# Kernel tuning notes

Measured on AMD Instinct MI355X. Metric: run time of the kernel, lower is better.

The kernel has to match this reference:

```python
import jax, jax.numpy as jnp
import numpy as np

B, W, F, N = 256, 512, 512, 512


def setup_inputs() -> dict:
    key = jax.random.key(0)
    k1, k2, k3, k4, k5 = jax.random.split(key, 5)
    return {
        "x": jax.random.normal(k1, (B, W, F), dtype=jnp.float32),
        "weight_k": jax.random.normal(k2, (F, N), dtype=jnp.float32),
        "weight_q": jax.random.normal(k3, (F, N), dtype=jnp.float32),
        "weight_v": jax.random.normal(k4, (F, N), dtype=jnp.float32),
        "w": jax.random.normal(k5, (W, 1), dtype=jnp.float32),
    }


def reference(x, weight_k, weight_q, weight_v, w):
    # x: (B, W, F)
    n_outputs = weight_k.shape[-1]
    # Per-word K/V projections (original loops over words; here one batched GEMM)
    K = jnp.einsum("bwf,fn->bwn", x, weight_k)  # (B, W, N)
    V = jnp.einsum("bwf,fn->bwn", x, weight_v)  # (B, W, N)
    # Per-sample query: t = x^T @ w -> (F,), q = t @ weight_q -> (N,)
    t = jnp.einsum("bwf,w->bf", x, w[:, 0])     # (B, F)
    Q = t @ weight_q                              # (B, N)
    # Scores over words, scaled, softmax across the word axis
    scores = jnp.einsum("bn,bwn->bw", Q, K) / jnp.sqrt(jnp.float32(n_outputs))
    weights = jax.nn.softmax(scores, axis=1)      # (B, W)
    # Weighted sum of V over words
    return jnp.einsum("bw,bwn->bn", weights, V)   # (B, N)
```

## Files before the change

### kernel.cpp

```cpp
#include <hip/hip_runtime.h>
#include <math.h>

#define B 256
#define W 512
#define F 512
#define N 512
#define GPART 4
#define WPG (W / GPART)

__global__ __launch_bounds__(512) void tpart_kernel(
    const float* __restrict__ x,
    const float* __restrict__ wvec,
    float* __restrict__ t_part)
{
    const int blk = blockIdx.x;
    const int g   = blk & (GPART - 1);
    const int b   = blk >> 2;
    const int tid = threadIdx.x;
    const int ws  = tid >> 7;
    const int f4  = tid & 127;

    __shared__ float s_w[WPG];
    __shared__ float s_part[4][F];

    if (tid < WPG) s_w[tid] = wvec[g * WPG + tid];
    __syncthreads();

    const float* xb = x + (size_t)b * W * F + (size_t)(g * WPG + ws * 32) * F;
    float4 acc = make_float4(0.f, 0.f, 0.f, 0.f);
#pragma unroll 8
    for (int i = 0; i < 32; ++i) {
        const float4 xv = *(const float4*)(xb + (size_t)i * F + f4 * 4);
        const float  ww = s_w[ws * 32 + i];
        acc.x += xv.x * ww; acc.y += xv.y * ww;
        acc.z += xv.z * ww; acc.w += xv.w * ww;
    }
    *(float4*)&s_part[ws][f4 * 4] = acc;
    __syncthreads();

    const float t = (s_part[0][tid] + s_part[1][tid])
                  + (s_part[2][tid] + s_part[3][tid]);
    t_part[(size_t)blk * F + tid] = t;
}

__global__ __launch_bounds__(512) void qr_kernel(
    const float* __restrict__ t_part,
    const float* __restrict__ Wq,
    const float* __restrict__ Wk,
    float* __restrict__ r_out)
{
    __shared__ float s_t[F];
    __shared__ float s_q[N];
    const int b = blockIdx.x, tid = threadIdx.x;

    float t = 0.f;
#pragma unroll
    for (int g = 0; g < GPART; ++g)
        t += t_part[((size_t)b * GPART + g) * F + tid];
    s_t[tid] = t;
    __syncthreads();

    float q0 = 0.f, q1 = 0.f, q2 = 0.f, q3 = 0.f;
#pragma unroll 4
    for (int f = 0; f < F; f += 4) {
        q0 += s_t[f + 0] * Wq[(size_t)(f + 0) * N + tid];
        q1 += s_t[f + 1] * Wq[(size_t)(f + 1) * N + tid];
        q2 += s_t[f + 2] * Wq[(size_t)(f + 2) * N + tid];
        q3 += s_t[f + 3] * Wq[(size_t)(f + 3) * N + tid];
    }
    s_q[tid] = (q0 + q1) + (q2 + q3);
    __syncthreads();

    const float4* wkrow = (const float4*)(Wk + (size_t)tid * N);
    float r0 = 0.f, r1 = 0.f, r2 = 0.f, r3 = 0.f;
#pragma unroll 8
    for (int n4 = 0; n4 < N / 4; ++n4) {
        const float4 kv = wkrow[n4];
        const float4 qv = *(const float4*)&s_q[n4 * 4];
        r0 += kv.x * qv.x; r1 += kv.y * qv.y;
        r2 += kv.z * qv.z; r3 += kv.w * qv.w;
    }
    r_out[(size_t)b * F + tid] =
        ((r0 + r1) + (r2 + r3)) * 0.04419417382415922f;
}

__global__ __launch_bounds__(512) void attn_kernel(
    const float* __restrict__ x,
    const float* __restrict__ Wv,
    const float* __restrict__ r_in,
    float* __restrict__ out)
{
    const int b    = blockIdx.x;
    const int tid  = threadIdx.x;
    const int lane = tid & 63;
    const int wv   = tid >> 6;

    __shared__ float s_c[8][F];
    __shared__ float s_m[8];
    __shared__ float s_l[8];
    __shared__ float s_cf[F];

    const float* xb = x + (size_t)b * W * F;
    const float* rb = r_in + (size_t)b * F;
    const float4 r0 = *(const float4*)(rb + lane * 4);
    const float4 r1 = *(const float4*)(rb + 256 + lane * 4);

    float m = -INFINITY, l = 0.f;
    float4 c0 = make_float4(0.f, 0.f, 0.f, 0.f);
    float4 c1 = make_float4(0.f, 0.f, 0.f, 0.f);

#pragma unroll 2
    for (int i = 0; i < 64; i += 2) {
        const float* rowA = xb + (size_t)(wv * 64 + i) * F;
        const float* rowB = rowA + F;
        const float4 a0 = *(const float4*)(rowA + lane * 4);
        const float4 a1 = *(const float4*)(rowA + 256 + lane * 4);
        const float4 b0 = *(const float4*)(rowB + lane * 4);
        const float4 b1 = *(const float4*)(rowB + 256 + lane * 4);

        float dA = a0.x * r0.x + a0.y * r0.y + a0.z * r0.z + a0.w * r0.w
                 + a1.x * r1.x + a1.y * r1.y + a1.z * r1.z + a1.w * r1.w;
        float dB = b0.x * r0.x + b0.y * r0.y + b0.z * r0.z + b0.w * r0.w
                 + b1.x * r1.x + b1.y * r1.y + b1.z * r1.z + b1.w * r1.w;
#pragma unroll
        for (int off = 32; off >= 1; off >>= 1) {
            dA += __shfl_xor(dA, off, 64);
            dB += __shfl_xor(dB, off, 64);
        }

        float mn = fmaxf(m, dA);
        float sc = __expf(m - mn);
        float p  = __expf(dA - mn);
        l = l * sc + p;
        c0.x = c0.x * sc + p * a0.x; c0.y = c0.y * sc + p * a0.y;
        c0.z = c0.z * sc + p * a0.z; c0.w = c0.w * sc + p * a0.w;
        c1.x = c1.x * sc + p * a1.x; c1.y = c1.y * sc + p * a1.y;
        c1.z = c1.z * sc + p * a1.z; c1.w = c1.w * sc + p * a1.w;
        m = mn;

        mn = fmaxf(m, dB);
        sc = __expf(m - mn);
        p  = __expf(dB - mn);
        l = l * sc + p;
        c0.x = c0.x * sc + p * b0.x; c0.y = c0.y * sc + p * b0.y;
        c0.z = c0.z * sc + p * b0.z; c0.w = c0.w * sc + p * b0.w;
        c1.x = c1.x * sc + p * b1.x; c1.y = c1.y * sc + p * b1.y;
        c1.z = c1.z * sc + p * b1.z; c1.w = c1.w * sc + p * b1.w;
        m = mn;
    }

    *(float4*)&s_c[wv][lane * 4]       = c0;
    *(float4*)&s_c[wv][256 + lane * 4] = c1;
    if (lane == 0) { s_m[wv] = m; s_l[wv] = l; }
    __syncthreads();

    float M = -INFINITY;
#pragma unroll
    for (int j = 0; j < 8; ++j) M = fmaxf(M, s_m[j]);
    float L = 0.f;
    float alpha[8];
#pragma unroll
    for (int j = 0; j < 8; ++j) {
        alpha[j] = __expf(s_m[j] - M);
        L += alpha[j] * s_l[j];
    }
    const float invL = 1.f / L;

    float cf = 0.f;
#pragma unroll
    for (int j = 0; j < 8; ++j) cf += alpha[j] * s_c[j][tid];
    s_cf[tid] = cf * invL;
    __syncthreads();

    float o0 = 0.f, o1 = 0.f, o2 = 0.f, o3 = 0.f;
#pragma unroll 4
    for (int f = 0; f < F; f += 4) {
        o0 += s_cf[f + 0] * Wv[(size_t)(f + 0) * N + tid];
        o1 += s_cf[f + 1] * Wv[(size_t)(f + 1) * N + tid];
        o2 += s_cf[f + 2] * Wv[(size_t)(f + 2) * N + tid];
        o3 += s_cf[f + 3] * Wv[(size_t)(f + 3) * N + tid];
    }
    out[(size_t)b * N + tid] = (o0 + o1) + (o2 + o3);
}

extern "C" void kernel_launch(void* const* d_in, const int* in_sizes, int n_in,
                              void* d_out, int out_size, void* d_ws, size_t ws_size,
                              hipStream_t stream)
{
    const float* x    = (const float*)d_in[0];
    const float* Wk   = (const float*)d_in[1];
    const float* Wq   = (const float*)d_in[2];
    const float* Wv   = (const float*)d_in[3];
    const float* wvec = (const float*)d_in[4];
    float* out    = (float*)d_out;
    float* t_part = (float*)d_ws;
    float* r      = t_part + (size_t)B * GPART * F;

    tpart_kernel<<<B * GPART, 512, 0, stream>>>(x, wvec, t_part);
    qr_kernel<<<B, 512, 0, stream>>>(t_part, Wq, Wk, r);
    attn_kernel<<<B, 512, 0, stream>>>(x, Wv, r, out);
}
```

Measured before the change: 465.6 us.

## Split attention over word quarters with partial softmax merge kernel

Attention is now split across four blocks per batch, each covering 128 words and emitting a partial max, sum and context vector. A new merge kernel combines the four partials with a log-sum-exp rescale and applies the Wv projection. The intent is more blocks in flight so the stream over x hides memory latency better. The cost is one extra launch and a small round trip of partial results through workspace memory.

```diff
diff --git a/kernel.cpp b/kernel.cpp
--- a/kernel.cpp
+++ b/kernel.cpp
@@ -84,13 +84,16 @@
         ((r0 + r1) + (r2 + r3)) * 0.04419417382415922f;
 }
 
-__global__ __launch_bounds__(512) void attn_kernel(
+__global__ __launch_bounds__(512, 8) void attn_part_kernel(
     const float* __restrict__ x,
-    const float* __restrict__ Wv,
     const float* __restrict__ r_in,
-    float* __restrict__ out)
-{
-    const int b    = blockIdx.x;
+    float* __restrict__ m_out,
+    float* __restrict__ l_out,
+    float* __restrict__ c_out)
+{
+    const int blk  = blockIdx.x;
+    const int b    = blk >> 2;
+    const int wq   = blk & 3;
     const int tid  = threadIdx.x;
     const int lane = tid & 63;
     const int wv   = tid >> 6;
@@ -98,9 +101,8 @@
     __shared__ float s_c[8][F];
     __shared__ float s_m[8];
     __shared__ float s_l[8];
-    __shared__ float s_cf[F];
-
-    const float* xb = x + (size_t)b * W * F;
+
+    const float* xb = x + (size_t)b * W * F + (size_t)(wq * 128) * F;
     const float* rb = r_in + (size_t)b * F;
     const float4 r0 = *(const float4*)(rb + lane * 4);
     const float4 r1 = *(const float4*)(rb + 256 + lane * 4);
@@ -110,8 +112,8 @@
     float4 c1 = make_float4(0.f, 0.f, 0.f, 0.f);
 
 #pragma unroll 2
-    for (int i = 0; i < 64; i += 2) {
-        const float* rowA = xb + (size_t)(wv * 64 + i) * F;
+    for (int i = 0; i < 16; i += 2) {
+        const float* rowA = xb + (size_t)(wv * 16 + i) * F;
         const float* rowB = rowA + F;
         const float4 a0 = *(const float4*)(rowA + lane * 4);
         const float4 a1 = *(const float4*)(rowA + 256 + lane * 4);
@@ -164,11 +166,44 @@
         alpha[j] = __expf(s_m[j] - M);
         L += alpha[j] * s_l[j];
     }
+
+    float cb = 0.f;
+#pragma unroll
+    for (int j = 0; j < 8; ++j) cb += alpha[j] * s_c[j][tid];
+    c_out[(size_t)blk * F + tid] = cb;
+    if (tid == 0) { m_out[blk] = M; l_out[blk] = L; }
+}
+
+__global__ __launch_bounds__(512) void merge_out_kernel(
+    const float* __restrict__ m_in,
+    const float* __restrict__ l_in,
+    const float* __restrict__ c_in,
+    const float* __restrict__ Wv,
+    float* __restrict__ out)
+{
+    __shared__ float s_cf[F];
+    const int b = blockIdx.x, tid = threadIdx.x;
+
+    float m4[4], l4[4];
+#pragma unroll
+    for (int j = 0; j < 4; ++j) {
+        m4[j] = m_in[b * 4 + j];
+        l4[j] = l_in[b * 4 + j];
+    }
+    float M = fmaxf(fmaxf(m4[0], m4[1]), fmaxf(m4[2], m4[3]));
+    float L = 0.f;
+    float alpha[4];
+#pragma unroll
+    for (int j = 0; j < 4; ++j) {
+        alpha[j] = __expf(m4[j] - M);
+        L += alpha[j] * l4[j];
+    }
     const float invL = 1.f / L;
 
     float cf = 0.f;
 #pragma unroll
-    for (int j = 0; j < 8; ++j) cf += alpha[j] * s_c[j][tid];
+    for (int j = 0; j < 4; ++j)
+        cf += alpha[j] * c_in[((size_t)b * 4 + j) * F + tid];
     s_cf[tid] = cf * invL;
     __syncthreads();
 
@@ -193,10 +228,15 @@
     const float* Wv   = (const float*)d_in[3];
     const float* wvec = (const float*)d_in[4];
     float* out    = (float*)d_out;
+
     float* t_part = (float*)d_ws;
-    float* r      = t_part + (size_t)B * GPART * F;
-
-    tpart_kernel<<<B * GPART, 512, 0, stream>>>(x, wvec, t_part);
+    float* r      = t_part + (size_t)B * 4 * F;
+    float* m_part = r + (size_t)B * F;
+    float* l_part = m_part + (size_t)B * 4;
+    float* c_part = l_part + (size_t)B * 4;
+
+    tpart_kernel<<<B * 4, 512, 0, stream>>>(x, wvec, t_part);
     qr_kernel<<<B, 512, 0, stream>>>(t_part, Wq, Wk, r);
-    attn_kernel<<<B, 512, 0, stream>>>(x, Wv, r, out);
-}
+    attn_part_kernel<<<B * 4, 512, 0, stream>>>(x, r, m_part, l_part, c_part);
+    merge_out_kernel<<<B, 512, 0, stream>>>(m_part, l_part, c_part, Wv, out);
+}
```

Result: slower. 476.7 us (+2.4%).
